# Optimization experiments

Hardware: AMD Instinct MI355X
Metric: run time of the kernel (lower is better)

The kernel has to match this reference:

```python
import jax, jax.numpy as jnp
import numpy as np

EPS = 1e-6
WINDOW = 1024  # config.sliding_window; mask: causal AND (q_idx - kv_idx < WINDOW)


def rms_norm(x, w=None):
    y = x * jax.lax.rsqrt(jnp.mean(jnp.square(x), axis=-1, keepdims=True) + EPS)
    return y * w if w is not None else y


def rotate_half(x):
    x1, x2 = jnp.split(x, 2, axis=-1)
    return jnp.concatenate([-x2, x1], axis=-1)


def apply_rope(x, cos, sin):
    # x: [B,S,H,D], cos/sin: [B,S,D] -> unsqueeze head dim (rotary_dim == D, x_pass empty)
    cos = cos[:, :, None, :]
    sin = sin[:, :, None, :]
    return x * cos + rotate_half(x) * sin


def setup_inputs() -> dict:
    key = jax.random.key(0)
    ks = jax.random.split(key, 8)
    B, S, HID, NH, NKV, D = 1, 2048, 2560, 8, 4, 256
    scale = 0.02
    hidden_states = jax.random.normal(ks[0], (B, S, HID), dtype=jnp.float32)
    wq = jax.random.normal(ks[1], (HID, NH * D), dtype=jnp.float32) * scale
    wk = jax.random.normal(ks[2], (HID, NKV * D), dtype=jnp.float32) * scale
    wv = jax.random.normal(ks[3], (HID, NKV * D), dtype=jnp.float32) * scale
    wo = jax.random.normal(ks[4], (NH * D, HID), dtype=jnp.float32) * scale
    q_norm_w = jnp.ones((D,), dtype=jnp.float32)
    k_norm_w = jnp.ones((D,), dtype=jnp.float32)
    # standard RoPE tables, rotary_dim = head_dim
    pos = jnp.arange(S, dtype=jnp.float32)
    inv_freq = 1.0 / (10000.0 ** (jnp.arange(0, D, 2, dtype=jnp.float32) / D))
    freqs = pos[:, None] * inv_freq[None, :]           # [S, D/2]
    emb = jnp.concatenate([freqs, freqs], axis=-1)     # [S, D]
    cos = jnp.cos(emb)[None]                           # [1, S, D]
    sin = jnp.sin(emb)[None]
    return dict(hidden_states=hidden_states, cos=cos, sin=sin,
                wq=wq, wk=wk, wv=wv, wo=wo,
                q_norm_w=q_norm_w, k_norm_w=k_norm_w)


def reference(hidden_states, cos, sin, wq, wk, wv, wo, q_norm_w, k_norm_w):
    B, S, _ = hidden_states.shape
    D = q_norm_w.shape[0]
    # projections -> [B,S,H,D]
    q = (hidden_states @ wq).reshape(B, S, -1, D)
    k = (hidden_states @ wk).reshape(B, S, -1, D)
    v = (hidden_states @ wv).reshape(B, S, -1, D)
    # QK-norm then RoPE (v gets non-affine RMSNorm)
    q = apply_rope(rms_norm(q, q_norm_w), cos, sin)
    k = apply_rope(rms_norm(k, k_norm_w), cos, sin)
    v = rms_norm(v)
    NH, NKV = q.shape[2], k.shape[2]
    rep = NH // NKV  # GQA: repeat KV heads
    k = jnp.repeat(k, rep, axis=2)
    v = jnp.repeat(v, rep, axis=2)
    # attention with scale=1.0 (QK-norm replaces 1/sqrt(d))
    scores = jnp.einsum('bqhd,bkhd->bhqk', q, k)
    qi = jnp.arange(S)[:, None]
    ki = jnp.arange(S)[None, :]
    mask = (ki <= qi) & (qi - ki < WINDOW)  # causal sliding window
    scores = jnp.where(mask[None, None], scores, -jnp.inf)
    attn = jax.nn.softmax(scores, axis=-1)
    out = jnp.einsum('bhqk,bkhd->bqhd', attn, v).reshape(B, S, -1)
    return out @ wo
```

## Files before the change

kernel.cpp:

```cpp
#include <hip/hip_runtime.h>
#include <hip/hip_bf16.h>
#include <math.h>

#define S_LEN 2048
#define HID 2560
#define NH 8
#define NKV 4
#define HD 256
#define WINDOW 1024

typedef short short8 __attribute__((ext_vector_type(8)));
typedef short short4_t __attribute__((ext_vector_type(4)));
typedef float f32x4 __attribute__((ext_vector_type(4)));
typedef float float4_t __attribute__((ext_vector_type(4)));

__device__ __forceinline__ short bf16_rne(float x) {
  unsigned u = __float_as_uint(x);
  return (short)((u + 0x7FFFu + ((u >> 16) & 1u)) >> 16);
}
__device__ __forceinline__ void split2(float x, short &h, short &l) {
  unsigned u = __float_as_uint(x);
  unsigned hb = (u + 0x7FFFu + ((u >> 16) & 1u)) & 0xFFFF0000u;
  h = (short)(hb >> 16);
  float r = x - __uint_as_float(hb);
  l = bf16_rne(r);
}

__device__ __forceinline__ void gload16(const short* g, short* l) {
  __builtin_amdgcn_global_load_lds(
      (const __attribute__((address_space(1))) void*)g,
      (__attribute__((address_space(3))) void*)l, 16, 0, 0);
}

#define SWZ(g, r) ((((g) ^ ((r) & 7))) * 8)
template <int MODE>
__global__ __launch_bounds__(256, 3)
void gemm_presplit(const short* __restrict__ Ah, const short* __restrict__ Al,
                   const short* __restrict__ Bh, const short* __restrict__ Bl,
                   float* __restrict__ C, int K, int ldc) {
  constexpr bool USE_AL = (MODE & 1) != 0;
  constexpr bool USE_BL = (MODE & 2) != 0;
  __shared__ short Ahs[64][64];
  __shared__ short Als[USE_AL ? 64 : 1][64];
  __shared__ short Bhs[128][64];
  __shared__ short Bls[USE_BL ? 128 : 1][64];
  const int tid = threadIdx.x;
  const int wv = tid >> 6, lane = tid & 63;
  const int wm = (wv >> 1) * 32, wn = (wv & 1) * 64;
  const int quad = lane >> 4, col = lane & 15;
  const int m0 = blockIdx.y * 64, n0 = blockIdx.x * 128;
  const int lr = lane >> 3;
  const size_t lgofs = (size_t)(((lane & 7) ^ lr)) * 8;
  const size_t aBase = (size_t)(m0 + lr) * K + lgofs;
  const size_t bBase = (size_t)(n0 + lr) * K + lgofs;

  f32x4 acc[2][4];
#pragma unroll
  for (int i = 0; i < 2; i++)
#pragma unroll
    for (int j = 0; j < 4; j++) acc[i][j] = (f32x4){0.f, 0.f, 0.f, 0.f};

  for (int k0 = 0; k0 < K; k0 += 64) {
#pragma unroll
    for (int c = wv; c < 8; c += 4) {
      const size_t go = aBase + (size_t)c * 8 * K + k0;
      gload16(Ah + go, &Ahs[c * 8][0]);
      if (USE_AL) gload16(Al + go, &Als[c * 8][0]);
    }
#pragma unroll
    for (int c = wv; c < 16; c += 4) {
      const size_t go = bBase + (size_t)c * 8 * K + k0;
      gload16(Bh + go, &Bhs[c * 8][0]);
      if (USE_BL) gload16(Bl + go, &Bls[c * 8][0]);
    }
    __syncthreads();
#pragma unroll
    for (int ks = 0; ks < 2; ks++) {
      const int g = ks * 4 + quad;
      short8 afh[2], afl[2], bfh[4], bfl[4];
#pragma unroll
      for (int i = 0; i < 2; i++) {
        int ar = wm + i * 16 + col;
        afh[i] = *reinterpret_cast<const short8*>(&Ahs[ar][SWZ(g, ar)]);
        if (USE_AL)
          afl[i] = *reinterpret_cast<const short8*>(&Als[ar][SWZ(g, ar)]);
      }
#pragma unroll
      for (int j = 0; j < 4; j++) {
        int br = wn + j * 16 + col;
        bfh[j] = *reinterpret_cast<const short8*>(&Bhs[br][SWZ(g, br)]);
        if (USE_BL)
          bfl[j] = *reinterpret_cast<const short8*>(&Bls[br][SWZ(g, br)]);
      }
#pragma unroll
      for (int i = 0; i < 2; i++)
#pragma unroll
        for (int j = 0; j < 4; j++) {
          acc[i][j] = __builtin_amdgcn_mfma_f32_16x16x32_bf16(afh[i], bfh[j], acc[i][j], 0, 0, 0);
          if (USE_BL)
            acc[i][j] = __builtin_amdgcn_mfma_f32_16x16x32_bf16(afh[i], bfl[j], acc[i][j], 0, 0, 0);
          if (USE_AL)
            acc[i][j] = __builtin_amdgcn_mfma_f32_16x16x32_bf16(afl[i], bfh[j], acc[i][j], 0, 0, 0);
        }
    }
    __syncthreads();
  }
#pragma unroll
  for (int i = 0; i < 2; i++)
#pragma unroll
    for (int j = 0; j < 4; j++)
#pragma unroll
      for (int r = 0; r < 4; r++)
        C[(size_t)(m0 + wm + i * 16 + quad * 4 + r) * ldc + n0 + wn + j * 16 + col] =
            acc[i][j][r];
}

__device__ __forceinline__ void wsplitT_body(const float* __restrict__ W,
                                             short* __restrict__ WTh,
                                             short* __restrict__ WTl,
                                             int KW, int NW, int n_ofs,
                                             int k0, int n0, int tid,
                                             float (*T)[65]) {
  const int r = tid >> 4, c4 = (tid & 15) * 4;
#pragma unroll
  for (int p = 0; p < 4; p++) {
    float4_t v = *reinterpret_cast<const float4_t*>(
        &W[(size_t)(k0 + r + p * 16) * NW + n0 + c4]);
#pragma unroll
    for (int e = 0; e < 4; e++) T[r + p * 16][c4 + e] = v[e];
  }
  __syncthreads();
  const int gk = tid & 7;
#pragma unroll
  for (int pass = 0; pass < 2; pass++) {
    const int n_loc = (tid >> 3) + pass * 32;
    short8 hv, lv;
#pragma unroll
    for (int e = 0; e < 8; e++) {
      short hh, ll;
      split2(T[gk * 8 + e][n_loc], hh, ll);
      hv[e] = hh; lv[e] = ll;
    }
    size_t base = (size_t)(n_ofs + n0 + n_loc) * KW + k0 + gk * 8;
    *reinterpret_cast<short8*>(WTh + base) = hv;
    *reinterpret_cast<short8*>(WTl + base) = lv;
  }
}

__global__ __launch_bounds__(256)
void prep_kernel(const float* __restrict__ hs, const float* __restrict__ wq,
                 const float* __restrict__ wk, const float* __restrict__ wv,
                 const float* __restrict__ wo, short* __restrict__ Ah,
                 short* __restrict__ Al, short* __restrict__ qkvTh,
                 short* __restrict__ qkvTl, short* __restrict__ woTh,
                 short* __restrict__ woTl) {
  __shared__ float T[64][65];
  const int bx = blockIdx.x;
  const int tid = threadIdx.x;
  if (bx < 5120) {
    const int i = bx * 256 + tid;
    float4_t v = reinterpret_cast<const float4_t*>(hs)[i];
    short4_t h, l;
#pragma unroll
    for (int e = 0; e < 4; e++) {
      short hh, ll;
      split2(v[e], hh, ll);
      h[e] = hh; l[e] = ll;
    }
    reinterpret_cast<short4_t*>(Ah)[i] = h;
    reinterpret_cast<short4_t*>(Al)[i] = l;
  } else if (bx < 6400) {
    const int local = bx - 5120;
    wsplitT_body(wq, qkvTh, qkvTl, HID, 2048, 0, (local % 40) * 64,
                 (local / 40) * 64, tid, T);
  } else if (bx < 7040) {
    const int local = bx - 6400;
    wsplitT_body(wk, qkvTh, qkvTl, HID, 1024, 2048, (local % 40) * 64,
                 (local / 40) * 64, tid, T);
  } else if (bx < 7680) {
    const int local = bx - 7040;
    wsplitT_body(wv, qkvTh, qkvTl, HID, 1024, 3072, (local % 40) * 64,
                 (local / 40) * 64, tid, T);
  } else {
    const int local = bx - 7680;
    wsplitT_body(wo, woTh, woTl, 2048, HID, 0, (local % 32) * 64,
                 (local / 32) * 64, tid, T);
  }
}

__global__ __launch_bounds__(256)
void norm_kernel(float* __restrict__ Cqkv, const float* __restrict__ qw,
                 const float* __restrict__ kw, const float* __restrict__ cosb,
                 const float* __restrict__ sinb, short* __restrict__ kh,
                 short* __restrict__ kl, short* __restrict__ vtb) {
  const int u = blockIdx.x & 15;
  const int sq = blockIdx.x >> 4;
  const int d = threadIdx.x;
  const int colbase = (u < 8) ? u * HD : (u < 12 ? 2048 + (u - 8) * HD
                                                 : 3072 + (u - 12) * HD);
  const size_t idx = (size_t)sq * 4096 + colbase + d;
  float x = Cqkv[idx];
  float v = x * x;
#pragma unroll
  for (int off = 32; off; off >>= 1) v += __shfl_down(v, off);
  __shared__ float red[4];
  __shared__ float sscale;
  __shared__ float nb[HD];
  if ((d & 63) == 0) red[d >> 6] = v;
  __syncthreads();
  if (d == 0)
    sscale = rsqrtf((red[0] + red[1] + red[2] + red[3]) * (1.0f / HD) + 1e-6f);
  __syncthreads();
  if (u < 12) {
    const float* w = (u < 8) ? qw : kw;
    float n = x * sscale * w[d];
    nb[d] = n;
    __syncthreads();
    float other = (d < HD / 2) ? -nb[d + HD / 2] : nb[d - HD / 2];
    n = n * cosb[(size_t)sq * HD + d] + other * sinb[(size_t)sq * HD + d];
    if (u < 8) {
      Cqkv[idx] = n;
    } else {
      short hh, ll;
      split2(n, hh, ll);
      const size_t b = ((size_t)sq * NKV + (u - 8)) * HD + d;
      kh[b] = hh;
      kl[b] = ll;
    }
  } else {
    vtb[((size_t)(u - 12) * HD + d) * S_LEN + sq] = bf16_rne(x * sscale);
  }
}

#define KSW(g, r) (((g) ^ ((r) & 7)) * 8)
#define VSW(g, d) ((((g) + ((d) >> 1)) & 3) * 8)
__global__ __launch_bounds__(256, 2)
void flash_attn2(const float* __restrict__ qn, int qrs,
                 const short* __restrict__ kh, const short* __restrict__ kl,
                 const short* __restrict__ vtb, float* __restrict__ oA,
                 float* __restrict__ oB, float* __restrict__ mlA,
                 float* __restrict__ mlB) {
  __shared__ short Kh[32][256], Kl[32][256];
  __shared__ short Vb[256][32];
  __shared__ short Ps[64][32];
  const int qt = blockIdx.x, h = blockIdx.y, sp = blockIdx.z;
  const int kvh = h >> 1;
  const int q0 = qt * 64;
  const int tid = threadIdx.x;
  const int w = tid >> 6, lane = tid & 63;
  const int quad = lane >> 4, col = lane & 15;
  float* oOut = sp ? oB : oA;
  float* mlOut = sp ? mlB : mlA;
  short8 qh[8], ql[8];
  {
    const float* qrow = qn + (size_t)(q0 + w * 16 + col) * qrs + h * HD;
#pragma unroll
    for (int s8 = 0; s8 < 8; s8++) {
      int d0 = s8 * 32 + quad * 8;
      float4_t a = *reinterpret_cast<const float4_t*>(qrow + d0);
      float4_t b = *reinterpret_cast<const float4_t*>(qrow + d0 + 4);
#pragma unroll
      for (int e = 0; e < 4; e++) {
        short hh, ll;
        split2(a[e], hh, ll);
        qh[s8][e] = hh; ql[s8][e] = ll;
        split2(b[e], hh, ll);
        qh[s8][4 + e] = hh; ql[s8][4 + e] = ll;
      }
    }
  }
  f32x4 o[16];
#pragma unroll
  for (int i = 0; i < 16; i++) o[i] = (f32x4){0.f, 0.f, 0.f, 0.f};
  float m_r[4] = {-INFINITY, -INFINITY, -INFINITY, -INFINITY};
  float l_r[4] = {0.f, 0.f, 0.f, 0.f};
  const int lo_t = (q0 > 1023) ? ((q0 - 1023) >> 5) : 0;
  const int hi_t = (q0 + 63) >> 5;
  const int halfn = (hi_t - lo_t + 2) >> 1;
  const int t0 = sp ? (lo_t + halfn) : lo_t;
  const int t1 = sp ? hi_t : (lo_t + halfn - 1);
  for (int kt = t0; kt <= t1; kt++) {
    const int kt0 = kt << 5;
    __syncthreads();
#pragma unroll
    for (int i = 0; i < 4; i++) {
      int idx = tid + i * 256;
      int row = idx >> 5, g = idx & 31;
      size_t gofs = ((size_t)(kt0 + row) * NKV + kvh) * HD + g * 8;
      *reinterpret_cast<short8*>(&Kh[row][KSW(g, row)]) =
          *reinterpret_cast<const short8*>(kh + gofs);
      *reinterpret_cast<short8*>(&Kl[row][KSW(g, row)]) =
          *reinterpret_cast<const short8*>(kl + gofs);
    }
#pragma unroll
    for (int i = 0; i < 4; i++) {
      int idx = tid + i * 256;
      int d = idx >> 2, g = idx & 3;
      *reinterpret_cast<short8*>(&Vb[d][VSW(g, d)]) =
          *reinterpret_cast<const short8*>(
              vtb + ((size_t)kvh * HD + d) * S_LEN + kt0 + g * 8);
    }
    __syncthreads();
    f32x4 sc[2];
    sc[0] = (f32x4){0.f, 0.f, 0.f, 0.f};
    sc[1] = (f32x4){0.f, 0.f, 0.f, 0.f};
#pragma unroll
    for (int s8 = 0; s8 < 8; s8++) {
#pragma unroll
      for (int nt = 0; nt < 2; nt++) {
        const int br = nt * 16 + col;
        const short8 bh = *reinterpret_cast<const short8*>(
            &Kh[br][KSW(s8 * 4 + quad, br)]);
        const short8 bl = *reinterpret_cast<const short8*>(
            &Kl[br][KSW(s8 * 4 + quad, br)]);
        sc[nt] = __builtin_amdgcn_mfma_f32_16x16x32_bf16(qh[s8], bh, sc[nt], 0, 0, 0);
        sc[nt] = __builtin_amdgcn_mfma_f32_16x16x32_bf16(qh[s8], bl, sc[nt], 0, 0, 0);
        sc[nt] = __builtin_amdgcn_mfma_f32_16x16x32_bf16(ql[s8], bh, sc[nt], 0, 0, 0);
      }
    }
#pragma unroll
    for (int r = 0; r < 4; r++) {
      const int q_abs = q0 + w * 16 + quad * 4 + r;
      const int prow = w * 16 + quad * 4 + r;
#pragma unroll
      for (int nt = 0; nt < 2; nt++) {
        int k_abs = kt0 + nt * 16 + col;
        bool valid = (k_abs <= q_abs) && (q_abs - k_abs < WINDOW);
        if (!valid) sc[nt][r] = -INFINITY;
      }
      float mx = fmaxf(sc[0][r], sc[1][r]);
      mx = fmaxf(mx, __shfl_xor(mx, 1));
      mx = fmaxf(mx, __shfl_xor(mx, 2));
      mx = fmaxf(mx, __shfl_xor(mx, 4));
      mx = fmaxf(mx, __shfl_xor(mx, 8));
      float mn = fmaxf(m_r[r], mx);
      float alpha = (mn == -INFINITY) ? 1.f : __expf(m_r[r] - mn);
      m_r[r] = mn;
      float rsum = 0.f;
#pragma unroll
      for (int nt = 0; nt < 2; nt++) {
        float s = sc[nt][r];
        float e = (s == -INFINITY) ? 0.f : __expf(s - mn);
        rsum += e;
        int ge = nt * 2 + (col >> 3);
        Ps[prow][VSW(ge, prow) + (col & 7)] = bf16_rne(e);
      }
      rsum += __shfl_xor(rsum, 1);
      rsum += __shfl_xor(rsum, 2);
      rsum += __shfl_xor(rsum, 4);
      rsum += __shfl_xor(rsum, 8);
      l_r[r] = l_r[r] * alpha + rsum;
#pragma unroll
      for (int nt2 = 0; nt2 < 16; nt2++) o[nt2][r] *= alpha;
    }
    __syncthreads();
    {
      const int prow = w * 16 + col;
      const short8 pa = *reinterpret_cast<const short8*>(&Ps[prow][VSW(quad, prow)]);
#pragma unroll
      for (int nt = 0; nt < 16; nt++) {
        const int vr = nt * 16 + col;
        const short8 vb = *reinterpret_cast<const short8*>(&Vb[vr][VSW(quad, vr)]);
        o[nt] = __builtin_amdgcn_mfma_f32_16x16x32_bf16(pa, vb, o[nt], 0, 0, 0);
      }
    }
  }
#pragma unroll
  for (int r = 0; r < 4; r++) {
    const int row = q0 + w * 16 + quad * 4 + r;
    const size_t base = ((size_t)row * NH + h) * HD;
#pragma unroll
    for (int nt = 0; nt < 16; nt++) oOut[base + nt * 16 + col] = o[nt][r];
    if (col == 0) {
      mlOut[((size_t)row * NH + h) * 2] = m_r[r];
      mlOut[((size_t)row * NH + h) * 2 + 1] = l_r[r];
    }
  }
}

__global__ __launch_bounds__(256)
void combine_kernel(const float* __restrict__ oA, const float* __restrict__ oB,
                    const float* __restrict__ mlA, const float* __restrict__ mlB,
                    short* __restrict__ ctxh) {
  const int idx = blockIdx.x;
  const int d = threadIdx.x;
  const float mA = mlA[(size_t)idx * 2], lA = mlA[(size_t)idx * 2 + 1];
  const float mB = mlB[(size_t)idx * 2], lB = mlB[(size_t)idx * 2 + 1];
  const float m = fmaxf(mA, mB);
  const float eA = (mA == -INFINITY) ? 0.f : __expf(mA - m);
  const float eB = (mB == -INFINITY) ? 0.f : __expf(mB - m);
  const float inv = 1.0f / (eA * lA + eB * lB);
  const size_t b = (size_t)idx * HD + d;
  ctxh[b] = bf16_rne((eA * oA[b] + eB * oB[b]) * inv);
}

extern "C" void kernel_launch(void* const* d_in, const int* in_sizes, int n_in,
                              void* d_out, int out_size, void* d_ws, size_t ws_size,
                              hipStream_t stream) {
  const float* hs   = (const float*)d_in[0];
  const float* cosb = (const float*)d_in[1];
  const float* sinb = (const float*)d_in[2];
  const float* wq   = (const float*)d_in[3];
  const float* wk   = (const float*)d_in[4];
  const float* wv   = (const float*)d_in[5];
  const float* wo   = (const float*)d_in[6];
  const float* qw   = (const float*)d_in[7];
  const float* kw   = (const float*)d_in[8];
  dim3 blk(256);

  const size_t szAh   = (size_t)S_LEN * HID * 2;
  const size_t szQKVT = (size_t)4096 * HID * 2;
  const size_t szWoT  = (size_t)HID * 2048 * 2;
  const size_t szCqkv = (size_t)S_LEN * 4096 * 4;
  const size_t szKh   = (size_t)S_LEN * NKV * HD * 2;
  const size_t szMl   = (size_t)S_LEN * NH * 2 * 4;

  char* p = (char*)d_ws + 256;
  short* Ah    = (short*)p;  p += szAh;
  short* Al    = (short*)p;  p += szAh;
  short* qkvTh = (short*)p;  p += szQKVT;
  short* qkvTl = (short*)p;  p += szQKVT;
  short* woTh  = (short*)p;  p += szWoT;
  short* woTl  = (short*)p;  p += szWoT;
  float* Cqkv  = (float*)p;  p += szCqkv;
  short* kh    = (short*)p;  p += szKh;
  short* kl    = (short*)p;  p += szKh;
  short* vtb   = (short*)p;  p += szKh;
  float* mlA   = (float*)p;  p += szMl;
  float* mlB   = (float*)p;  p += szMl;
  float* oA    = (float*)Ah;
  float* oB    = (float*)d_out;
  short* ctxh  = qkvTh;

  prep_kernel<<<8960, blk, 0, stream>>>(hs, wq, wk, wv, wo, Ah, Al, qkvTh,
                                        qkvTl, woTh, woTl);
  gemm_presplit<3><<<dim3(3072 / 128, S_LEN / 64), blk, 0, stream>>>(
      Ah, Al, qkvTh, qkvTl, Cqkv, HID, 4096);
  gemm_presplit<2><<<dim3(1024 / 128, S_LEN / 64), blk, 0, stream>>>(
      Ah, Al, qkvTh + (size_t)3072 * HID, qkvTl + (size_t)3072 * HID,
      Cqkv + 3072, HID, 4096);
  norm_kernel<<<S_LEN * 16, blk, 0, stream>>>(Cqkv, qw, kw, cosb, sinb, kh, kl,
                                              vtb);
  flash_attn2<<<dim3(S_LEN / 64, NH, 2), blk, 0, stream>>>(
      Cqkv, 4096, kh, kl, vtb, oA, oB, mlA, mlB);
  combine_kernel<<<S_LEN * NH, blk, 0, stream>>>(oA, oB, mlA, mlB, ctxh);
  gemm_presplit<2><<<dim3(HID / 128, S_LEN / 64), blk, 0, stream>>>(
      ctxh, ctxh, woTh, woTl, (float*)d_out, 2048, HID);
}
```

Before: 444.2 us.

## Merge QKV GEMM launches and fuse Q RMSNorm+RoPE into attention prologue

Combines the two QKV projection GEMM launches into one kernel that dispatches by block index, so the Q/K and V tiles share a single grid. Moves the Q-side RMSNorm and RoPE out of norm_kernel and into the flash-attention Q load, which computes the row norm with cross-lane shuffles and applies the rotation in registers. This halves norm_kernel's grid and drops a full read-modify-write of Q in global memory. The cost is that the norm and rotation for each Q row are recomputed by both KV-split blocks, and the attention prologue holds more registers.

```diff
diff --git a/kernel.cpp b/kernel.cpp
--- a/kernel.cpp
+++ b/kernel.cpp
@@ -34,21 +34,17 @@
 
 #define SWZ(g, r) ((((g) ^ ((r) & 7))) * 8)
 template <int MODE>
-__global__ __launch_bounds__(256, 3)
-void gemm_presplit(const short* __restrict__ Ah, const short* __restrict__ Al,
-                   const short* __restrict__ Bh, const short* __restrict__ Bl,
-                   float* __restrict__ C, int K, int ldc) {
+__device__ __forceinline__ void gemm_body(
+    const short* __restrict__ Ah, const short* __restrict__ Al,
+    const short* __restrict__ Bh, const short* __restrict__ Bl,
+    float* __restrict__ C, int K, int ldc, int m0, int n0, int tid,
+    short (*__restrict__ Ahs)[64], short (*__restrict__ Als)[64],
+    short (*__restrict__ Bhs)[64], short (*__restrict__ Bls)[64]) {
   constexpr bool USE_AL = (MODE & 1) != 0;
   constexpr bool USE_BL = (MODE & 2) != 0;
-  __shared__ short Ahs[64][64];
-  __shared__ short Als[USE_AL ? 64 : 1][64];
-  __shared__ short Bhs[128][64];
-  __shared__ short Bls[USE_BL ? 128 : 1][64];
-  const int tid = threadIdx.x;
   const int wv = tid >> 6, lane = tid & 63;
   const int wm = (wv >> 1) * 32, wn = (wv & 1) * 64;
   const int quad = lane >> 4, col = lane & 15;
-  const int m0 = blockIdx.y * 64, n0 = blockIdx.x * 128;
   const int lr = lane >> 3;
   const size_t lgofs = (size_t)(((lane & 7) ^ lr)) * 8;
   const size_t aBase = (size_t)(m0 + lr) * K + lgofs;
@@ -113,6 +109,39 @@
       for (int r = 0; r < 4; r++)
         C[(size_t)(m0 + wm + i * 16 + quad * 4 + r) * ldc + n0 + wn + j * 16 + col] =
             acc[i][j][r];
+}
+
+template <int MODE>
+__global__ __launch_bounds__(256, 3)
+void gemm_presplit(const short* __restrict__ Ah, const short* __restrict__ Al,
+                   const short* __restrict__ Bh, const short* __restrict__ Bl,
+                   float* __restrict__ C, int K, int ldc) {
+  __shared__ short Ahs[64][64];
+  __shared__ short Als[(MODE & 1) ? 64 : 1][64];
+  __shared__ short Bhs[128][64];
+  __shared__ short Bls[(MODE & 2) ? 128 : 1][64];
+  gemm_body<MODE>(Ah, Al, Bh, Bl, C, K, ldc, blockIdx.y * 64, blockIdx.x * 128,
+                  threadIdx.x, Ahs, Als, Bhs, Bls);
+}
+
+__global__ __launch_bounds__(256, 3)
+void gemm_qkv(const short* __restrict__ Ah, const short* __restrict__ Al,
+              const short* __restrict__ qkvTh, const short* __restrict__ qkvTl,
+              float* __restrict__ Cqkv) {
+  __shared__ short Ahs[64][64];
+  __shared__ short Als[64][64];
+  __shared__ short Bhs[128][64];
+  __shared__ short Bls[128][64];
+  const int b = blockIdx.x;
+  if (b < 768) {
+    gemm_body<3>(Ah, Al, qkvTh, qkvTl, Cqkv, HID, 4096, (b / 24) * 64,
+                 (b % 24) * 128, threadIdx.x, Ahs, Als, Bhs, Bls);
+  } else {
+    const int t = b - 768;
+    gemm_body<2>(Ah, Al, qkvTh + (size_t)3072 * HID, qkvTl + (size_t)3072 * HID,
+                 Cqkv + 3072, HID, 4096, (t / 8) * 64, (t % 8) * 128,
+                 threadIdx.x, Ahs, Als, Bhs, Bls);
+  }
 }
 
 __device__ __forceinline__ void wsplitT_body(const float* __restrict__ W,
@@ -189,15 +218,14 @@
 }
 
 __global__ __launch_bounds__(256)
-void norm_kernel(float* __restrict__ Cqkv, const float* __restrict__ qw,
-                 const float* __restrict__ kw, const float* __restrict__ cosb,
-                 const float* __restrict__ sinb, short* __restrict__ kh,
-                 short* __restrict__ kl, short* __restrict__ vtb) {
-  const int u = blockIdx.x & 15;
-  const int sq = blockIdx.x >> 4;
+void norm_kernel(const float* __restrict__ Cqkv, const float* __restrict__ kw,
+                 const float* __restrict__ cosb, const float* __restrict__ sinb,
+                 short* __restrict__ kh, short* __restrict__ kl,
+                 short* __restrict__ vtb) {
+  const int u = blockIdx.x & 7;
+  const int sq = blockIdx.x >> 3;
   const int d = threadIdx.x;
-  const int colbase = (u < 8) ? u * HD : (u < 12 ? 2048 + (u - 8) * HD
-                                                 : 3072 + (u - 12) * HD);
+  const int colbase = (u < 4) ? 2048 + u * HD : 3072 + (u - 4) * HD;
   const size_t idx = (size_t)sq * 4096 + colbase + d;
   float x = Cqkv[idx];
   float v = x * x;
@@ -211,24 +239,19 @@
   if (d == 0)
     sscale = rsqrtf((red[0] + red[1] + red[2] + red[3]) * (1.0f / HD) + 1e-6f);
   __syncthreads();
-  if (u < 12) {
-    const float* w = (u < 8) ? qw : kw;
-    float n = x * sscale * w[d];
+  if (u < 4) {
+    float n = x * sscale * kw[d];
     nb[d] = n;
     __syncthreads();
     float other = (d < HD / 2) ? -nb[d + HD / 2] : nb[d - HD / 2];
     n = n * cosb[(size_t)sq * HD + d] + other * sinb[(size_t)sq * HD + d];
-    if (u < 8) {
-      Cqkv[idx] = n;
-    } else {
-      short hh, ll;
-      split2(n, hh, ll);
-      const size_t b = ((size_t)sq * NKV + (u - 8)) * HD + d;
-      kh[b] = hh;
-      kl[b] = ll;
-    }
+    short hh, ll;
+    split2(n, hh, ll);
+    const size_t b = ((size_t)sq * NKV + u) * HD + d;
+    kh[b] = hh;
+    kl[b] = ll;
   } else {
-    vtb[((size_t)(u - 12) * HD + d) * S_LEN + sq] = bf16_rne(x * sscale);
+    vtb[((size_t)(u - 4) * HD + d) * S_LEN + sq] = bf16_rne(x * sscale);
   }
 }
 
@@ -236,6 +259,8 @@
 #define VSW(g, d) ((((g) + ((d) >> 1)) & 3) * 8)
 __global__ __launch_bounds__(256, 2)
 void flash_attn2(const float* __restrict__ qn, int qrs,
+                 const float* __restrict__ qw, const float* __restrict__ cosb,
+                 const float* __restrict__ sinb,
                  const short* __restrict__ kh, const short* __restrict__ kl,
                  const short* __restrict__ vtb, float* __restrict__ oA,
                  float* __restrict__ oB, float* __restrict__ mlA,
@@ -253,18 +278,53 @@
   float* mlOut = sp ? mlB : mlA;
   short8 qh[8], ql[8];
   {
-    const float* qrow = qn + (size_t)(q0 + w * 16 + col) * qrs + h * HD;
+    const int sq = q0 + w * 16 + col;
+    const float* qrow = qn + (size_t)sq * qrs + h * HD;
+    float xq[8][8];
+    float ssum = 0.f;
 #pragma unroll
     for (int s8 = 0; s8 < 8; s8++) {
-      int d0 = s8 * 32 + quad * 8;
+      const int d0 = s8 * 32 + quad * 8;
       float4_t a = *reinterpret_cast<const float4_t*>(qrow + d0);
       float4_t b = *reinterpret_cast<const float4_t*>(qrow + d0 + 4);
 #pragma unroll
       for (int e = 0; e < 4; e++) {
+        xq[s8][e] = a[e];
+        xq[s8][4 + e] = b[e];
+        ssum += a[e] * a[e] + b[e] * b[e];
+      }
+    }
+    ssum += __shfl_xor(ssum, 16);
+    ssum += __shfl_xor(ssum, 32);
+    const float scale = rsqrtf(ssum * (1.0f / HD) + 1e-6f);
+#pragma unroll
+    for (int s8 = 0; s8 < 8; s8++) {
+      const int d0 = s8 * 32 + quad * 8;
+      float4_t w0 = *reinterpret_cast<const float4_t*>(qw + d0);
+      float4_t w1 = *reinterpret_cast<const float4_t*>(qw + d0 + 4);
+#pragma unroll
+      for (int e = 0; e < 4; e++) {
+        xq[s8][e] *= scale * w0[e];
+        xq[s8][4 + e] *= scale * w1[e];
+      }
+    }
+    const float* crow = cosb + (size_t)sq * HD;
+    const float* srow = sinb + (size_t)sq * HD;
+#pragma unroll
+    for (int s8 = 0; s8 < 8; s8++) {
+      const int d0 = s8 * 32 + quad * 8;
+      float4_t c0 = *reinterpret_cast<const float4_t*>(crow + d0);
+      float4_t c1 = *reinterpret_cast<const float4_t*>(crow + d0 + 4);
+      float4_t s0 = *reinterpret_cast<const float4_t*>(srow + d0);
+      float4_t s1 = *reinterpret_cast<const float4_t*>(srow + d0 + 4);
+      const float sgn = (s8 < 4) ? -1.f : 1.f;
+      const int pp = s8 ^ 4;
+#pragma unroll
+      for (int e = 0; e < 4; e++) {
         short hh, ll;
-        split2(a[e], hh, ll);
+        split2(xq[s8][e] * c0[e] + sgn * xq[pp][e] * s0[e], hh, ll);
         qh[s8][e] = hh; ql[s8][e] = ll;
-        split2(b[e], hh, ll);
+        split2(xq[s8][4 + e] * c1[e] + sgn * xq[pp][4 + e] * s1[e], hh, ll);
         qh[s8][4 + e] = hh; ql[s8][4 + e] = ll;
       }
     }
@@ -434,15 +494,10 @@
 
   prep_kernel<<<8960, blk, 0, stream>>>(hs, wq, wk, wv, wo, Ah, Al, qkvTh,
                                         qkvTl, woTh, woTl);
-  gemm_presplit<3><<<dim3(3072 / 128, S_LEN / 64), blk, 0, stream>>>(
-      Ah, Al, qkvTh, qkvTl, Cqkv, HID, 4096);
-  gemm_presplit<2><<<dim3(1024 / 128, S_LEN / 64), blk, 0, stream>>>(
-      Ah, Al, qkvTh + (size_t)3072 * HID, qkvTl + (size_t)3072 * HID,
-      Cqkv + 3072, HID, 4096);
-  norm_kernel<<<S_LEN * 16, blk, 0, stream>>>(Cqkv, qw, kw, cosb, sinb, kh, kl,
-                                              vtb);
+  gemm_qkv<<<1024, blk, 0, stream>>>(Ah, Al, qkvTh, qkvTl, Cqkv);
+  norm_kernel<<<S_LEN * 8, blk, 0, stream>>>(Cqkv, kw, cosb, sinb, kh, kl, vtb);
   flash_attn2<<<dim3(S_LEN / 64, NH, 2), blk, 0, stream>>>(
-      Cqkv, 4096, kh, kl, vtb, oA, oB, mlA, mlB);
+      Cqkv, 4096, qw, cosb, sinb, kh, kl, vtb, oA, oB, mlA, mlB);
   combine_kernel<<<S_LEN * NH, blk, 0, stream>>>(oA, oB, mlA, mlB, ctxh);
   gemm_presplit<2><<<dim3(HID / 128, S_LEN / 64), blk, 0, stream>>>(
       ctxh, ctxh, woTh, woTl, (float*)d_out, 2048, HID);
```

Measured after the change: 417.4 us. 1.06x faster.
